# Performance work log

Measured on AMD Instinct MI355X. Metric: run time of the kernel, lower is better.

## Reference

```python
import jax, jax.numpy as jnp
import numpy as np

N, A, C = 65536, 512, 1000


def setup_inputs() -> dict:
    key = jax.random.key(0)
    k1, k2, k3, k4, k5 = jax.random.split(key, 5)
    return {
        "features": jax.random.normal(k1, (N, A), dtype=jnp.float32),
        "labels": jax.random.randint(k2, (N,), 0, C),
        "count": jax.random.uniform(k3, (C,), dtype=jnp.float32) * 100.0,
        "mean": jax.random.normal(k4, (C, A), dtype=jnp.float32),
        "cov": jax.random.uniform(k5, (C, A), dtype=jnp.float32),
    }


def reference(features, labels, count, mean, cov):
    # Per-class counts and feature sums via segment reduction (math identical to
    # the torch onehot-expand NxCxA construction, but O(N*A) instead of O(N*C*A)).
    c = count.shape[0]
    ones = jnp.ones((features.shape[0],), dtype=features.dtype)
    n_c = jax.ops.segment_sum(ones, labels, num_segments=c)            # [C]
    sums = jax.ops.segment_sum(features, labels, num_segments=c)      # [C, A]
    amt = jnp.where(n_c == 0, 1.0, n_c)                                # Amount_CxA (zeros -> 1)
    ave = sums / amt[:, None]                                          # ave_CxA
    diff = features - ave[labels]                                      # onehot*(x - ave) per row
    var = jax.ops.segment_sum(diff * diff, labels, num_segments=c) / amt[:, None]
    # EMA blend weight; torch sets NaN (0/0) entries to 0.
    denom = n_c + count
    w = jnp.where(denom == 0, 0.0, n_c / jnp.where(denom == 0, 1.0, denom))[:, None]  # [C,1]
    cov_new = cov * (1.0 - w) + var * w + w * (1.0 - w) * (mean - ave) ** 2
    mean_new = mean * (1.0 - w) + ave * w
    count_new = count + n_c
    return cov_new, mean_new, count_new
```

## Files before the change

kernel.cpp:

```cpp
#include <hip/hip_runtime.h>

constexpr int N_ROWS   = 65536;
constexpr int N_FEAT   = 512;
constexpr int N_FEAT4  = N_FEAT / 4;
constexpr int N_CLS    = 1000;

constexpr int CAP        = 256;
constexpr int CNT_STRIDE = 16;
constexpr int LIST_CAP   = 2048;

__device__ __forceinline__ void gather_finish(
    const float* __restrict__ features, const int* list, const int n,
    const float* __restrict__ count,
    const float* __restrict__ cls_mean,
    const float* __restrict__ cls_cov,
    float*       __restrict__ out,
    const int c, const int t, float4* red_s, float4* red_q)
{
    const int half = t >> 7;
    const int col  = t & 127;
    const float4* __restrict__ f4 = (const float4*)features;

    float s0 = 0.f, s1 = 0.f, s2 = 0.f, s3 = 0.f;
    float q0 = 0.f, q1 = 0.f, q2 = 0.f, q3 = 0.f;

    #define ACC(v) \
        s0 += v.x; q0 = fmaf(v.x, v.x, q0); \
        s1 += v.y; q1 = fmaf(v.y, v.y, q1); \
        s2 += v.z; q2 = fmaf(v.z, v.z, q2); \
        s3 += v.w; q3 = fmaf(v.w, v.w, q3);

    int j = 0;
    for (; j + 16 <= n; j += 16) {
        const int r0 = list[j +  0 + half], r1 = list[j +  2 + half];
        const int r2 = list[j +  4 + half], r3 = list[j +  6 + half];
        const int r4 = list[j +  8 + half], r5 = list[j + 10 + half];
        const int r6 = list[j + 12 + half], r7 = list[j + 14 + half];
        const float4 v0 = f4[(size_t)r0 * N_FEAT4 + col];
        const float4 v1 = f4[(size_t)r1 * N_FEAT4 + col];
        const float4 v2 = f4[(size_t)r2 * N_FEAT4 + col];
        const float4 v3 = f4[(size_t)r3 * N_FEAT4 + col];
        const float4 v4 = f4[(size_t)r4 * N_FEAT4 + col];
        const float4 v5 = f4[(size_t)r5 * N_FEAT4 + col];
        const float4 v6 = f4[(size_t)r6 * N_FEAT4 + col];
        const float4 v7 = f4[(size_t)r7 * N_FEAT4 + col];
        ACC(v0) ACC(v1) ACC(v2) ACC(v3) ACC(v4) ACC(v5) ACC(v6) ACC(v7)
    }
    for (; j + 8 <= n; j += 8) {
        const int r0 = list[j + 0 + half], r1 = list[j + 2 + half];
        const int r2 = list[j + 4 + half], r3 = list[j + 6 + half];
        const float4 v0 = f4[(size_t)r0 * N_FEAT4 + col];
        const float4 v1 = f4[(size_t)r1 * N_FEAT4 + col];
        const float4 v2 = f4[(size_t)r2 * N_FEAT4 + col];
        const float4 v3 = f4[(size_t)r3 * N_FEAT4 + col];
        ACC(v0) ACC(v1) ACC(v2) ACC(v3)
    }
    if (j < n) {
        #pragma unroll
        for (int u = 0; u < 4; ++u) {
            const int idx = j + 2 * u + half;
            const int r = (idx < n) ? list[idx] : 0;
            const float w = (idx < n) ? 1.f : 0.f;
            const float4 v = f4[(size_t)r * N_FEAT4 + col];
            const float vx = v.x * w, vy = v.y * w, vz = v.z * w, vw = v.w * w;
            s0 += vx; q0 = fmaf(vx, v.x, q0);
            s1 += vy; q1 = fmaf(vy, v.y, q1);
            s2 += vz; q2 = fmaf(vz, v.z, q2);
            s3 += vw; q3 = fmaf(vw, v.w, q3);
        }
    }
    #undef ACC

    __syncthreads();
    if (half == 1) {
        red_s[col] = make_float4(s0, s1, s2, s3);
        red_q[col] = make_float4(q0, q1, q2, q3);
    }
    __syncthreads();
    if (half == 0) {
        const float4 rs = red_s[col], rq = red_q[col];
        s0 += rs.x; s1 += rs.y; s2 += rs.z; s3 += rs.w;
        q0 += rq.x; q1 += rq.y; q2 += rq.z; q3 += rq.w;

        const float fn  = (float)n;
        const float amt = (n > 0) ? fn : 1.0f;
        const float inv = 1.0f / amt;
        const float a0 = s0 * inv, a1 = s1 * inv, a2 = s2 * inv, a3 = s3 * inv;
        const float vr0 = q0 * inv - a0 * a0;
        const float vr1 = q1 * inv - a1 * a1;
        const float vr2 = q2 * inv - a2 * a2;
        const float vr3 = q3 * inv - a3 * a3;

        const float cnt_c = count[c];
        const float denom = fn + cnt_c;
        const float w     = (denom == 0.f) ? 0.f : fn / denom;
        const float omw   = 1.0f - w;

        const float4 mv = ((const float4*)cls_mean)[c * N_FEAT4 + col];
        const float4 cv = ((const float4*)cls_cov)[c * N_FEAT4 + col];
        const float d0 = mv.x - a0, d1 = mv.y - a1, d2 = mv.z - a2, d3 = mv.w - a3;

        float4 covn, meann;
        covn.x  = cv.x * omw + vr0 * w + w * omw * d0 * d0;
        covn.y  = cv.y * omw + vr1 * w + w * omw * d1 * d1;
        covn.z  = cv.z * omw + vr2 * w + w * omw * d2 * d2;
        covn.w  = cv.w * omw + vr3 * w + w * omw * d3 * d3;
        meann.x = mv.x * omw + a0 * w;
        meann.y = mv.y * omw + a1 * w;
        meann.z = mv.z * omw + a2 * w;
        meann.w = mv.w * omw + a3 * w;

        ((float4*)out)[c * N_FEAT4 + col] = covn;
        ((float4*)(out + N_CLS * N_FEAT))[c * N_FEAT4 + col] = meann;
        if (t == 0) out[2 * N_CLS * N_FEAT + c] = cnt_c + fn;
    }
}

__global__ __launch_bounds__(256) void bin_rows(const int* __restrict__ labels,
                                                int* __restrict__ ws)
{
    const int i   = blockIdx.x * 256 + threadIdx.x;
    const int lab = labels[i];
    const int pos = atomicAdd(&ws[lab * CNT_STRIDE], 1);
    if (pos < CAP) ws[N_CLS * CNT_STRIDE + lab * CAP + pos] = i;
}

__global__ __launch_bounds__(256) void estimator_main(
    const float* __restrict__ features,
    const int*   __restrict__ ws,
    const float* __restrict__ count,
    const float* __restrict__ cls_mean,
    const float* __restrict__ cls_cov,
    float*       __restrict__ out)
{
    const int c = blockIdx.x;
    const int t = threadIdx.x;

    __shared__ int slist[CAP];
    __shared__ float4 red_s[128];
    __shared__ float4 red_q[128];

    const int n = min(ws[c * CNT_STRIDE], CAP);
    const int* __restrict__ gl = ws + N_CLS * CNT_STRIDE + c * CAP;
    if (t < n) slist[t] = gl[t];
    __syncthreads();

    gather_finish(features, slist, n, count, cls_mean, cls_cov, out, c, t,
                  red_s, red_q);
}

__global__ __launch_bounds__(256) void estimator_onepass(
    const float* __restrict__ features,
    const int*   __restrict__ labels,
    const float* __restrict__ count,
    const float* __restrict__ cls_mean,
    const float* __restrict__ cls_cov,
    float*       __restrict__ out)
{
    const int c = blockIdx.x;
    const int t = threadIdx.x;
    const int wave = t >> 6;
    const int lane = t & 63;

    __shared__ int cnt;
    __shared__ int list[LIST_CAP];
    __shared__ float4 red_s[128];
    __shared__ float4 red_q[128];

    if (t == 0) cnt = 0;
    __syncthreads();

    {
        const int4* __restrict__ l4 = (const int4*)labels;
        const int waveBase4 = wave * 4096;
        for (int s = 0; s < 16; ++s) {
            const int base4 = waveBase4 + s * 256 + lane;
            const int4 va = l4[base4];
            const int4 vb = l4[base4 + 64];
            const int4 vc = l4[base4 + 128];
            const int4 vd = l4[base4 + 192];
            unsigned mask = 0;
            mask |= (va.x == c) ? 0x0001u : 0u; mask |= (va.y == c) ? 0x0002u : 0u;
            mask |= (va.z == c) ? 0x0004u : 0u; mask |= (va.w == c) ? 0x0008u : 0u;
            mask |= (vb.x == c) ? 0x0010u : 0u; mask |= (vb.y == c) ? 0x0020u : 0u;
            mask |= (vb.z == c) ? 0x0040u : 0u; mask |= (vb.w == c) ? 0x0080u : 0u;
            mask |= (vc.x == c) ? 0x0100u : 0u; mask |= (vc.y == c) ? 0x0200u : 0u;
            mask |= (vc.z == c) ? 0x0400u : 0u; mask |= (vc.w == c) ? 0x0800u : 0u;
            mask |= (vd.x == c) ? 0x1000u : 0u; mask |= (vd.y == c) ? 0x2000u : 0u;
            mask |= (vd.z == c) ? 0x4000u : 0u; mask |= (vd.w == c) ? 0x8000u : 0u;

            const int m = __popc(mask);
            int inc = m;
            #pragma unroll
            for (int d = 1; d < 64; d <<= 1) {
                const int x = __shfl_up(inc, d, 64);
                if (lane >= d) inc += x;
            }
            int basep = 0;
            if (lane == 63) basep = atomicAdd(&cnt, inc);
            basep = __shfl(basep, 63, 64);
            int off = basep + inc - m;
            unsigned mm = mask;
            while (mm) {
                const int k = __ffs(mm) - 1; mm &= mm - 1;
                const int row = (base4 + (k >> 2) * 64) * 4 + (k & 3);
                if (off < LIST_CAP) list[off] = row;
                ++off;
            }
        }
    }
    __syncthreads();
    const int n = min(cnt, LIST_CAP);

    gather_finish(features, list, n, count, cls_mean, cls_cov, out, c, t,
                  red_s, red_q);
}

extern "C" void kernel_launch(void* const* d_in, const int* in_sizes, int n_in,
                              void* d_out, int out_size, void* d_ws, size_t ws_size,
                              hipStream_t stream) {
    const float* features = (const float*)d_in[0];
    const int*   labels   = (const int*)d_in[1];
    const float* count    = (const float*)d_in[2];
    const float* mean     = (const float*)d_in[3];
    const float* cov      = (const float*)d_in[4];
    float* out = (float*)d_out;

    const size_t ws_need =
        ((size_t)N_CLS * CNT_STRIDE + (size_t)N_CLS * CAP) * sizeof(int);

    if (d_ws != nullptr && ws_size >= ws_need) {
        int* ws = (int*)d_ws;
        hipMemsetAsync(ws, 0, (size_t)N_CLS * CNT_STRIDE * sizeof(int), stream);
        bin_rows<<<N_ROWS / 256, 256, 0, stream>>>(labels, ws);
        estimator_main<<<N_CLS, 256, 0, stream>>>(features, ws, count, mean, cov, out);
    } else {
        estimator_onepass<<<N_CLS, 256, 0, stream>>>(features, labels, count,
                                                     mean, cov, out);
    }
}
```

Baseline: 209.5 us.

## Fuse count reset, row binning and per-class reduction into one cooperative kernel

Replaces the memset, the binning kernel and the main kernel with one cooperatively launched kernel. Inside it, grid-wide syncs separate three phases: zeroing the class counters, atomically binning row indices per class, and the per-class gather/reduce/EMA update. The aim is to remove the separate launches and the gaps between them. In exchange it pays for two grid barriers and needs all 1000 blocks co-resident, which the launch bounds of 4 blocks per CU are set to allow. If the cooperative launch fails it falls back to the old three-step path.

```diff
diff --git a/kernel.cpp b/kernel.cpp
--- a/kernel.cpp
+++ b/kernel.cpp
@@ -1,4 +1,7 @@
 #include <hip/hip_runtime.h>
+#include <hip/hip_cooperative_groups.h>
+
+namespace cg = cooperative_groups;
 
 constexpr int N_ROWS   = 65536;
 constexpr int N_FEAT   = 512;
@@ -114,6 +117,46 @@
         ((float4*)(out + N_CLS * N_FEAT))[c * N_FEAT4 + col] = meann;
         if (t == 0) out[2 * N_CLS * N_FEAT + c] = cnt_c + fn;
     }
+}
+
+__global__ __launch_bounds__(256, 4) void estimator_fused(
+    const float* __restrict__ features,
+    const int*   __restrict__ labels,
+    const float* __restrict__ count,
+    const float* __restrict__ cls_mean,
+    const float* __restrict__ cls_cov,
+    float*       __restrict__ out,
+    int*         __restrict__ ws)
+{
+    const int c   = blockIdx.x;
+    const int t   = threadIdx.x;
+    const int tid = c * 256 + t;
+
+    cg::grid_group grid = cg::this_grid();
+
+    if (tid < N_CLS) ws[tid * CNT_STRIDE] = 0;
+    __threadfence();
+    grid.sync();
+
+    if (tid < N_ROWS) {
+        const int lab = labels[tid];
+        const int pos = atomicAdd(&ws[lab * CNT_STRIDE], 1);
+        if (pos < CAP) ws[N_CLS * CNT_STRIDE + lab * CAP + pos] = tid;
+    }
+    __threadfence();
+    grid.sync();
+
+    __shared__ int slist[CAP];
+    __shared__ float4 red_s[128];
+    __shared__ float4 red_q[128];
+
+    const int n = min(ws[c * CNT_STRIDE], CAP);
+    const int* __restrict__ gl = ws + N_CLS * CNT_STRIDE + c * CAP;
+    if (t < n) slist[t] = gl[t];
+    __syncthreads();
+
+    gather_finish(features, slist, n, count, cls_mean, cls_cov, out, c, t,
+                  red_s, red_q);
 }
 
 __global__ __launch_bounds__(256) void bin_rows(const int* __restrict__ labels,
@@ -231,9 +274,21 @@
 
     if (d_ws != nullptr && ws_size >= ws_need) {
         int* ws = (int*)d_ws;
-        hipMemsetAsync(ws, 0, (size_t)N_CLS * CNT_STRIDE * sizeof(int), stream);
-        bin_rows<<<N_ROWS / 256, 256, 0, stream>>>(labels, ws);
-        estimator_main<<<N_CLS, 256, 0, stream>>>(features, ws, count, mean, cov, out);
+
+        void* args[] = {
+            (void*)&features, (void*)&labels, (void*)&count,
+            (void*)&mean, (void*)&cov, (void*)&out, (void*)&ws
+        };
+        hipError_t err = hipLaunchCooperativeKernel(
+            (const void*)estimator_fused, dim3(N_CLS), dim3(256), args, 0, stream);
+
+        if (err != hipSuccess) {
+            (void)hipGetLastError();
+            hipMemsetAsync(ws, 0, (size_t)N_CLS * CNT_STRIDE * sizeof(int), stream);
+            bin_rows<<<N_ROWS / 256, 256, 0, stream>>>(labels, ws);
+            estimator_main<<<N_CLS, 256, 0, stream>>>(features, ws, count, mean,
+                                                      cov, out);
+        }
     } else {
         estimator_onepass<<<N_CLS, 256, 0, stream>>>(features, labels, count,
                                                      mean, cov, out);
```

Result: slower. 491.2 us (+134.4%).

## Replace global-atomic row binning with per-block class scans, drop memset

Applied to the files above, without the earlier changes.

Row binning now uses 250 blocks. Each block scans the whole label array and collects rows for its 4 classes with shared-memory atomics, then writes compacted lists and counts, so the memset and the global atomics are no longer needed. Feature gathers switch to nontemporal loads, and the per-class mean, cov and count loads are moved ahead of the accumulation loop so they overlap with it. The cost is that every bin block rereads the full 256KB label array, and row order within each list is no longer deterministic.

```diff
diff --git a/kernel.cpp b/kernel.cpp
--- a/kernel.cpp
+++ b/kernel.cpp
@@ -8,6 +8,11 @@
 constexpr int CAP        = 256;
 constexpr int CNT_STRIDE = 16;
 constexpr int LIST_CAP   = 2048;
+
+constexpr int CLS_PER_BLK = 4;
+constexpr int BIN_BLOCKS  = N_CLS / CLS_PER_BLK;
+
+typedef float f32x4 __attribute__((ext_vector_type(4)));
 
 __device__ __forceinline__ void gather_finish(
     const float* __restrict__ features, const int* list, const int n,
@@ -19,7 +24,15 @@
 {
     const int half = t >> 7;
     const int col  = t & 127;
-    const float4* __restrict__ f4 = (const float4*)features;
+    const f32x4* __restrict__ f4 = (const f32x4*)features;
+
+    float cnt_c = 0.f;
+    f32x4 mv = {0.f, 0.f, 0.f, 0.f}, cv = {0.f, 0.f, 0.f, 0.f};
+    if (half == 0) {
+        cnt_c = count[c];
+        mv = ((const f32x4*)cls_mean)[c * N_FEAT4 + col];
+        cv = ((const f32x4*)cls_cov)[c * N_FEAT4 + col];
+    }
 
     float s0 = 0.f, s1 = 0.f, s2 = 0.f, s3 = 0.f;
     float q0 = 0.f, q1 = 0.f, q2 = 0.f, q3 = 0.f;
@@ -36,23 +49,23 @@
         const int r2 = list[j +  4 + half], r3 = list[j +  6 + half];
         const int r4 = list[j +  8 + half], r5 = list[j + 10 + half];
         const int r6 = list[j + 12 + half], r7 = list[j + 14 + half];
-        const float4 v0 = f4[(size_t)r0 * N_FEAT4 + col];
-        const float4 v1 = f4[(size_t)r1 * N_FEAT4 + col];
-        const float4 v2 = f4[(size_t)r2 * N_FEAT4 + col];
-        const float4 v3 = f4[(size_t)r3 * N_FEAT4 + col];
-        const float4 v4 = f4[(size_t)r4 * N_FEAT4 + col];
-        const float4 v5 = f4[(size_t)r5 * N_FEAT4 + col];
-        const float4 v6 = f4[(size_t)r6 * N_FEAT4 + col];
-        const float4 v7 = f4[(size_t)r7 * N_FEAT4 + col];
+        const f32x4 v0 = __builtin_nontemporal_load(&f4[(size_t)r0 * N_FEAT4 + col]);
+        const f32x4 v1 = __builtin_nontemporal_load(&f4[(size_t)r1 * N_FEAT4 + col]);
+        const f32x4 v2 = __builtin_nontemporal_load(&f4[(size_t)r2 * N_FEAT4 + col]);
+        const f32x4 v3 = __builtin_nontemporal_load(&f4[(size_t)r3 * N_FEAT4 + col]);
+        const f32x4 v4 = __builtin_nontemporal_load(&f4[(size_t)r4 * N_FEAT4 + col]);
+        const f32x4 v5 = __builtin_nontemporal_load(&f4[(size_t)r5 * N_FEAT4 + col]);
+        const f32x4 v6 = __builtin_nontemporal_load(&f4[(size_t)r6 * N_FEAT4 + col]);
+        const f32x4 v7 = __builtin_nontemporal_load(&f4[(size_t)r7 * N_FEAT4 + col]);
         ACC(v0) ACC(v1) ACC(v2) ACC(v3) ACC(v4) ACC(v5) ACC(v6) ACC(v7)
     }
     for (; j + 8 <= n; j += 8) {
         const int r0 = list[j + 0 + half], r1 = list[j + 2 + half];
         const int r2 = list[j + 4 + half], r3 = list[j + 6 + half];
-        const float4 v0 = f4[(size_t)r0 * N_FEAT4 + col];
-        const float4 v1 = f4[(size_t)r1 * N_FEAT4 + col];
-        const float4 v2 = f4[(size_t)r2 * N_FEAT4 + col];
-        const float4 v3 = f4[(size_t)r3 * N_FEAT4 + col];
+        const f32x4 v0 = __builtin_nontemporal_load(&f4[(size_t)r0 * N_FEAT4 + col]);
+        const f32x4 v1 = __builtin_nontemporal_load(&f4[(size_t)r1 * N_FEAT4 + col]);
+        const f32x4 v2 = __builtin_nontemporal_load(&f4[(size_t)r2 * N_FEAT4 + col]);
+        const f32x4 v3 = __builtin_nontemporal_load(&f4[(size_t)r3 * N_FEAT4 + col]);
         ACC(v0) ACC(v1) ACC(v2) ACC(v3)
     }
     if (j < n) {
@@ -61,7 +74,7 @@
             const int idx = j + 2 * u + half;
             const int r = (idx < n) ? list[idx] : 0;
             const float w = (idx < n) ? 1.f : 0.f;
-            const float4 v = f4[(size_t)r * N_FEAT4 + col];
+            const f32x4 v = __builtin_nontemporal_load(&f4[(size_t)r * N_FEAT4 + col]);
             const float vx = v.x * w, vy = v.y * w, vz = v.z * w, vw = v.w * w;
             s0 += vx; q0 = fmaf(vx, v.x, q0);
             s1 += vy; q1 = fmaf(vy, v.y, q1);
@@ -91,13 +104,10 @@
         const float vr2 = q2 * inv - a2 * a2;
         const float vr3 = q3 * inv - a3 * a3;
 
-        const float cnt_c = count[c];
         const float denom = fn + cnt_c;
         const float w     = (denom == 0.f) ? 0.f : fn / denom;
         const float omw   = 1.0f - w;
 
-        const float4 mv = ((const float4*)cls_mean)[c * N_FEAT4 + col];
-        const float4 cv = ((const float4*)cls_cov)[c * N_FEAT4 + col];
         const float d0 = mv.x - a0, d1 = mv.y - a1, d2 = mv.z - a2, d3 = mv.w - a3;
 
         float4 covn, meann;
@@ -116,13 +126,43 @@
     }
 }
 
-__global__ __launch_bounds__(256) void bin_rows(const int* __restrict__ labels,
-                                                int* __restrict__ ws)
-{
-    const int i   = blockIdx.x * 256 + threadIdx.x;
-    const int lab = labels[i];
-    const int pos = atomicAdd(&ws[lab * CNT_STRIDE], 1);
-    if (pos < CAP) ws[N_CLS * CNT_STRIDE + lab * CAP + pos] = i;
+__global__ __launch_bounds__(256) void bin_by_class(const int* __restrict__ labels,
+                                                    int* __restrict__ ws)
+{
+    const int b  = blockIdx.x;
+    const int t  = threadIdx.x;
+    const int c0 = b * CLS_PER_BLK;
+
+    __shared__ int cnt[CLS_PER_BLK];
+    __shared__ int lst[CLS_PER_BLK][CAP];
+
+    if (t < CLS_PER_BLK) cnt[t] = 0;
+    __syncthreads();
+
+    const int4* __restrict__ l4 = (const int4*)labels;
+    #pragma unroll 4
+    for (int s = 0; s < 64; ++s) {
+        const int i4  = s * 256 + t;
+        const int4 v  = l4[i4];
+        const int row = i4 * 4;
+        unsigned d;
+        d = (unsigned)(v.x - c0);
+        if (d < CLS_PER_BLK) { const int p = atomicAdd(&cnt[d], 1); if (p < CAP) lst[d][p] = row;     }
+        d = (unsigned)(v.y - c0);
+        if (d < CLS_PER_BLK) { const int p = atomicAdd(&cnt[d], 1); if (p < CAP) lst[d][p] = row + 1; }
+        d = (unsigned)(v.z - c0);
+        if (d < CLS_PER_BLK) { const int p = atomicAdd(&cnt[d], 1); if (p < CAP) lst[d][p] = row + 2; }
+        d = (unsigned)(v.w - c0);
+        if (d < CLS_PER_BLK) { const int p = atomicAdd(&cnt[d], 1); if (p < CAP) lst[d][p] = row + 3; }
+    }
+    __syncthreads();
+
+    if (t < CLS_PER_BLK) ws[(c0 + t) * CNT_STRIDE] = min(cnt[t], CAP);
+    #pragma unroll
+    for (int d = 0; d < CLS_PER_BLK; ++d) {
+        const int n = min(cnt[d], CAP);
+        if (t < n) ws[N_CLS * CNT_STRIDE + (c0 + d) * CAP + t] = lst[d][t];
+    }
 }
 
 __global__ __launch_bounds__(256) void estimator_main(
@@ -231,9 +271,9 @@
 
     if (d_ws != nullptr && ws_size >= ws_need) {
         int* ws = (int*)d_ws;
-        hipMemsetAsync(ws, 0, (size_t)N_CLS * CNT_STRIDE * sizeof(int), stream);
-        bin_rows<<<N_ROWS / 256, 256, 0, stream>>>(labels, ws);
-        estimator_main<<<N_CLS, 256, 0, stream>>>(features, ws, count, mean, cov, out);
+        bin_by_class<<<BIN_BLOCKS, 256, 0, stream>>>(labels, ws);
+        estimator_main<<<N_CLS, 256, 0, stream>>>(features, ws, count, mean,
+                                                  cov, out);
     } else {
         estimator_onepass<<<N_CLS, 256, 0, stream>>>(features, labels, count,
                                                      mean, cov, out);
```

New measurement: 223.3 us. +6.6%, slower.
